# Performance work log

Measured on AMD Instinct MI355X. Metric: run time of the kernel, lower is better.

## Reference

```python
import jax, jax.numpy as jnp
import numpy as np

B, S, D = 4, 8192, 512


def log_g(x):
    # torch: where(x>=0, log(relu(x)+0.5), -softplus(-x)); relu(x)+0.5 >= 0.5 so log is safe
    return jnp.where(x >= 0, jnp.log(jax.nn.relu(x) + 0.5), -jax.nn.softplus(-x))


def parallel_scan_log(log_coeffs, log_values):
    # log_coeffs: (B,S,D); log_values: (B,S+1,D)
    a_star = jnp.pad(jnp.cumsum(log_coeffs, axis=1), ((0, 0), (1, 0), (0, 0)))  # (B,S+1,D)
    log_h = a_star + jax.lax.cumlogsumexp(log_values - a_star, axis=1)
    return jnp.exp(log_h)[:, 1:]  # (B,S,D)


def setup_inputs() -> dict:
    key = jax.random.key(0)
    ks = jax.random.split(key, 7)
    scale = 1.0 / np.sqrt(D)
    x = jax.random.normal(ks[0], (B, S, D), dtype=jnp.float32)
    pre_h = jnp.zeros((B, 1, D), dtype=jnp.float32)
    Wf = jax.random.normal(ks[1], (D, D), dtype=jnp.float32) * scale
    bf = jax.random.normal(ks[2], (D,), dtype=jnp.float32) * 0.01
    Wi = jax.random.normal(ks[3], (D, D), dtype=jnp.float32) * scale
    bi = jax.random.normal(ks[4], (D,), dtype=jnp.float32) * 0.01
    Wh = jax.random.normal(ks[5], (D, D), dtype=jnp.float32) * scale
    bh = jax.random.normal(ks[6], (D,), dtype=jnp.float32) * 0.01
    return {"x": x, "pre_h": pre_h, "Wf": Wf, "bf": bf, "Wi": Wi, "bi": bi, "Wh": Wh, "bh": bh}


def reference(x, pre_h, Wf, bf, Wi, bi, Wh, bh):
    # gates: log(sigmoid(k)) = -softplus(-k)
    log_f = -jax.nn.softplus(-(jnp.einsum('bsd,de->bse', x, Wf) + bf))
    log_i = -jax.nn.softplus(-(jnp.einsum('bsd,de->bse', x, Wi) + bi))
    log_tilde_h = log_g(jnp.einsum('bsd,de->bse', x, Wh) + bh)
    log_pre_h = log_g(pre_h)  # (B,1,D)
    log_values = jnp.concatenate([log_pre_h, log_i + log_tilde_h], axis=1)  # (B,S+1,D)
    return parallel_scan_log(log_f, log_values)
```

## Files before the change

### kernel.cpp

```cpp
#include <hip/hip_runtime.h>
#include <hip/hip_bf16.h>

#define BATCH 4
#define SEQ   8192
#define DIM   512
#define M_TOT (BATCH*SEQ)
#define NCHUNK 128
#define CLEN   64

#define GBM 128
#define GBN 128
#define GBK 64

typedef __attribute__((ext_vector_type(4))) int int4v;

__device__ __forceinline__ float sigmoidf_(float x) {
    return 1.0f / (1.0f + __expf(-x));
}
__device__ __forceinline__ float gfun_(float x) {
    return (x >= 0.0f) ? (x + 0.5f) : sigmoidf_(x);
}

__device__ __forceinline__ void stage16(const void* g, void* lds) {
    __builtin_amdgcn_global_load_lds((const __attribute__((address_space(1))) void*)g,
                                     (__attribute__((address_space(3))) void*)lds,
                                     16, 0, 0);
}

__global__ __launch_bounds__(256) void quant_x(const float* __restrict__ x,
                                               char* __restrict__ xh, char* __restrict__ xl)
{
    const int t = blockIdx.x * 256 + threadIdx.x;
    float4 v = ((const float4*)x)[t];
    float vals[4] = {v.x, v.y, v.z, v.w};
    char hs[4], ls[4];
    #pragma unroll
    for (int e = 0; e < 4; ++e) {
        float c = fminf(fmaxf(vals[e], -15.8f), 15.8f);
        int q = (int)rintf(c * 2048.0f);
        int hi = (q + 128) >> 8;
        int lo = q - (hi << 8);
        hs[e] = (char)hi; ls[e] = (char)lo;
    }
    char4 hv = {hs[0], hs[1], hs[2], hs[3]};
    char4 lv = {ls[0], ls[1], ls[2], ls[3]};
    *(char4*)&xh[(size_t)t * 4] = hv;
    *(char4*)&xl[(size_t)t * 4] = lv;
}

__global__ __launch_bounds__(256) void quant_wT(
    const float* __restrict__ Wf, const float* __restrict__ Wi, const float* __restrict__ Wh,
    char* __restrict__ wth, char* __restrict__ wtl)
{
    __shared__ float tile[64][65];
    const int g = blockIdx.z;
    const float* W = (g == 0) ? Wf : (g == 1) ? Wi : Wh;
    const int k0 = blockIdx.x * 64, n0 = blockIdx.y * 64;
    const int c = threadIdx.x & 63, r4 = threadIdx.x >> 6;
    #pragma unroll
    for (int p = 0; p < 16; ++p) {
        int r = p * 4 + r4;
        tile[r][c] = W[(size_t)(k0 + r) * DIM + n0 + c];
    }
    __syncthreads();
    const size_t gbase = (size_t)g * DIM * DIM;
    #pragma unroll
    for (int p = 0; p < 16; ++p) {
        int nr = p * 4 + r4;
        float w = tile[c][nr];
        float cl = fminf(fmaxf(w, -0.49f), 0.49f);
        int q = (int)rintf(cl * 65536.0f);
        int hi = (q + 128) >> 8;
        int lo = q - (hi << 8);
        size_t o = gbase + (size_t)(n0 + nr) * DIM + k0 + c;
        wth[o] = (char)hi;
        wtl[o] = (char)lo;
    }
}

__global__ __launch_bounds__(256, 2) void gemm_i8(
    const char* __restrict__ xh, const char* __restrict__ xl,
    const char* __restrict__ wth, const char* __restrict__ wtl,
    const float* __restrict__ bfv, const float* __restrict__ biv, const float* __restrict__ bhv,
    float* __restrict__ fb, float* __restrict__ sib, float* __restrict__ ghb)
{
    __shared__ char sA[2][GBM][GBK];
    __shared__ char sB[2][GBN][GBK];

    const int g  = blockIdx.x >> 2;
    const int n0 = (blockIdx.x & 3) * GBN;
    const int m0 = blockIdx.y * GBM;
    const int tid  = threadIdx.x;
    const int wave = tid >> 6;
    const int lane = tid & 63;
    const int wi = wave >> 1, wj = wave & 1;

    const char* wh_g = wth + (size_t)g * DIM * DIM;
    const char* wl_g = wtl + (size_t)g * DIM * DIM;

    int4v P2[4][4], P1[4][4];
    const int4v zero = {0, 0, 0, 0};
    #pragma unroll
    for (int i = 0; i < 4; ++i)
        #pragma unroll
        for (int j = 0; j < 4; ++j) { P2[i][j] = zero; P1[i][j] = zero; }

    for (int k0 = 0; k0 < DIM; k0 += GBK) {
        #pragma unroll
        for (int it = 0; it < 2; ++it) {
            const int grp = it * 4 + wave;
            const int m   = grp * 16 + (lane >> 2);
            const int kb  = (lane & 3) * 16;
            const int ksw = kb ^ (((m >> 1) & 3) << 4);
            char* ldsA = &sA[0][grp * 16][0];
            char* ldsB = &sB[0][grp * 16][0];
            char* ldsA1 = &sA[1][grp * 16][0];
            char* ldsB1 = &sB[1][grp * 16][0];
            stage16(xh  + (size_t)(m0 + m) * DIM + k0 + ksw, ldsA);
            stage16(xl  + (size_t)(m0 + m) * DIM + k0 + ksw, ldsA1);
            stage16(wh_g + (size_t)(n0 + m) * DIM + k0 + ksw, ldsB);
            stage16(wl_g + (size_t)(n0 + m) * DIM + k0 + ksw, ldsB1);
        }
        __syncthreads();

        const int kseg = (lane >> 4) * 16;
        int4v bhf[4], blf[4];
        #pragma unroll
        for (int j = 0; j < 4; ++j) {
            const int col = wj * 64 + j * 16 + (lane & 15);
            const int ks  = kseg ^ (((col >> 1) & 3) << 4);
            bhf[j] = *(const int4v*)&sB[0][col][ks];
            blf[j] = *(const int4v*)&sB[1][col][ks];
        }
        #pragma unroll
        for (int i = 0; i < 4; ++i) {
            const int row = wi * 64 + i * 16 + (lane & 15);
            const int ks  = kseg ^ (((row >> 1) & 3) << 4);
            int4v ahf = *(const int4v*)&sA[0][row][ks];
            int4v alf = *(const int4v*)&sA[1][row][ks];
            #pragma unroll
            for (int j = 0; j < 4; ++j) {
                P2[i][j] = __builtin_amdgcn_mfma_i32_16x16x64_i8(ahf, bhf[j], P2[i][j], 0, 0, 0);
                P1[i][j] = __builtin_amdgcn_mfma_i32_16x16x64_i8(ahf, blf[j], P1[i][j], 0, 0, 0);
                P1[i][j] = __builtin_amdgcn_mfma_i32_16x16x64_i8(alf, bhf[j], P1[i][j], 0, 0, 0);
            }
        }
        __syncthreads();
    }

    const float c2 = 1.0f / 2048.0f;
    const float c1 = 1.0f / 524288.0f;
    const float* bias = (g == 0) ? bfv : (g == 1) ? biv : bhv;
    float* outp = (g == 0) ? fb : (g == 1) ? sib : ghb;
    #pragma unroll
    for (int i = 0; i < 4; ++i) {
        #pragma unroll
        for (int j = 0; j < 4; ++j) {
            const int col = n0 + wj * 64 + j * 16 + (lane & 15);
            const float bv = bias[col];
            #pragma unroll
            for (int r = 0; r < 4; ++r) {
                const int row = m0 + wi * 64 + i * 16 + (lane >> 4) * 4 + r;
                float kv = (float)P2[i][j][r] * c2 + (float)P1[i][j][r] * c1 + bv;
                float o = (g == 2) ? gfun_(kv) : sigmoidf_(kv);
                outp[(size_t)row * DIM + col] = o;
            }
        }
    }
}

__global__ __launch_bounds__(256) void scan_pass1(
    const float* __restrict__ fb, const float* __restrict__ sib, const float* __restrict__ ghb,
    float* __restrict__ Ach, float* __restrict__ Bch)
{
    const int d = blockIdx.x * 256 + threadIdx.x;
    const int c = blockIdx.y;
    const int b = blockIdx.z;
    float A = 1.0f, Bacc = 0.0f;
    size_t base = ((size_t)(b * SEQ + c * CLEN)) * DIM + d;
    #pragma unroll 4
    for (int t = 0; t < CLEN; ++t) {
        float f = fb[base + (size_t)t * DIM];
        float v = sib[base + (size_t)t * DIM] * ghb[base + (size_t)t * DIM];
        Bacc = fmaf(f, Bacc, v);
        A *= f;
    }
    const int idx = (b * NCHUNK + c) * DIM + d;
    Ach[idx] = A;
    Bch[idx] = Bacc;
}

__global__ __launch_bounds__(256) void scan_pass2(
    const float* __restrict__ pre_h,
    const float* __restrict__ Ach, const float* __restrict__ Bch,
    float* __restrict__ carry)
{
    const int gidx = blockIdx.x * 256 + threadIdx.x;
    const int b = gidx >> 9;
    const int d = gidx & (DIM - 1);
    float h = gfun_(pre_h[b * DIM + d]);
    for (int c = 0; c < NCHUNK; ++c) {
        const int idx = (b * NCHUNK + c) * DIM + d;
        carry[idx] = h;
        h = fmaf(Ach[idx], h, Bch[idx]);
    }
}

__global__ __launch_bounds__(256) void scan_pass3(
    const float* __restrict__ fb, const float* __restrict__ sib, const float* __restrict__ ghb,
    const float* __restrict__ carry, float* __restrict__ out)
{
    const int d = blockIdx.x * 256 + threadIdx.x;
    const int c = blockIdx.y;
    const int b = blockIdx.z;
    float h = carry[(b * NCHUNK + c) * DIM + d];
    size_t base = ((size_t)(b * SEQ + c * CLEN)) * DIM + d;
    #pragma unroll 4
    for (int t = 0; t < CLEN; ++t) {
        float f = fb[base + (size_t)t * DIM];
        float v = sib[base + (size_t)t * DIM] * ghb[base + (size_t)t * DIM];
        h = fmaf(f, h, v);
        out[base + (size_t)t * DIM] = h;
    }
}

extern "C" void kernel_launch(void* const* d_in, const int* in_sizes, int n_in,
                              void* d_out, int out_size, void* d_ws, size_t ws_size,
                              hipStream_t stream) {
    const float* x     = (const float*)d_in[0];
    const float* pre_h = (const float*)d_in[1];
    const float* Wf    = (const float*)d_in[2];
    const float* bf    = (const float*)d_in[3];
    const float* Wi    = (const float*)d_in[4];
    const float* bi    = (const float*)d_in[5];
    const float* Wh    = (const float*)d_in[6];
    const float* bh    = (const float*)d_in[7];
    float* out = (float*)d_out;

    char* ws = (char*)d_ws;
    const size_t XQ = (size_t)M_TOT * DIM;
    const size_t WQ = (size_t)3 * DIM * DIM;
    const size_t FB = (size_t)M_TOT * DIM * sizeof(float);

    char*  xh  = ws;
    char*  xl  = ws + XQ;
    char*  wth = ws + 2 * XQ;
    char*  wtl = ws + 2 * XQ + WQ;
    float* fbuf  = (float*)(ws + 2 * XQ + 2 * WQ);
    float* sibuf = (float*)((char*)fbuf + FB);
    float* ghbuf = (float*)((char*)sibuf + FB);
    float* Ach   = (float*)((char*)ghbuf + FB);
    float* Bch   = (float*)((char*)Ach + (size_t)BATCH * NCHUNK * DIM * 4);
    float* carry = (float*)((char*)Bch + (size_t)BATCH * NCHUNK * DIM * 4);

    quant_x<<<(M_TOT * DIM / 4) / 256, 256, 0, stream>>>(x, xh, xl);
    quant_wT<<<dim3(8, 8, 3), 256, 0, stream>>>(Wf, Wi, Wh, wth, wtl);
    gemm_i8<<<dim3(12, M_TOT / GBM), 256, 0, stream>>>(
        xh, xl, wth, wtl, bf, bi, bh, fbuf, sibuf, ghbuf);
    scan_pass1<<<dim3(DIM / 256, NCHUNK, BATCH), 256, 0, stream>>>(fbuf, sibuf, ghbuf, Ach, Bch);
    scan_pass2<<<(BATCH * DIM) / 256, 256, 0, stream>>>(pre_h, Ach, Bch, carry);
    scan_pass3<<<dim3(DIM / 256, NCHUNK, BATCH), 256, 0, stream>>>(fbuf, sibuf, ghbuf, carry, out);
}
```

Measured before the change: 321.9 us.

## Fuse three gate GEMMs per tile and emit product buffer, double-buffer LDS

Each block now computes all three gate projections for one output tile in sequence. It keeps sigmoid(i) in registers and writes only f and the product v = sigmoid(i)*g(h) to global memory, so one full-size float intermediate buffer and its re-reads in both scan passes go away. The K loop gains LDS double buffering, with the next tile's global-to-LDS loads issued before the current tile's MFMAs, and a swizzled block index improves L2 reuse of X rows. In exchange, the 64 extra registers per thread may push register pressure past the 2-blocks-per-CU launch bound and cause spills. The LDS footprint also doubles to 64KB.

```diff
diff --git a/kernel.cpp b/kernel.cpp
--- a/kernel.cpp
+++ b/kernel.cpp
@@ -7,10 +7,6 @@
 #define M_TOT (BATCH*SEQ)
 #define NCHUNK 128
 #define CLEN   64
-
-#define GBM 128
-#define GBN 128
-#define GBK 64
 
 typedef __attribute__((ext_vector_type(4))) int int4v;
 
@@ -78,99 +74,129 @@
     }
 }
 
-__global__ __launch_bounds__(256, 2) void gemm_i8(
+__global__ __launch_bounds__(256, 2) void gemm_fused(
     const char* __restrict__ xh, const char* __restrict__ xl,
     const char* __restrict__ wth, const char* __restrict__ wtl,
     const float* __restrict__ bfv, const float* __restrict__ biv, const float* __restrict__ bhv,
-    float* __restrict__ fb, float* __restrict__ sib, float* __restrict__ ghb)
-{
-    __shared__ char sA[2][GBM][GBK];
-    __shared__ char sB[2][GBN][GBK];
-
-    const int g  = blockIdx.x >> 2;
-    const int n0 = (blockIdx.x & 3) * GBN;
-    const int m0 = blockIdx.y * GBM;
+    float* __restrict__ fb, float* __restrict__ vb)
+{
+    __shared__ char sA[2][2][128][64];
+    __shared__ char sB[2][2][128][64];
+
+    const int bid = blockIdx.x;
+    const int xr = bid & 7;
+    const int tt = bid >> 3;
+    const int n0 = (tt & 3) * 128;
+    const int m0 = (xr + 8 * (tt >> 2)) * 128;
+
     const int tid  = threadIdx.x;
     const int wave = tid >> 6;
     const int lane = tid & 63;
     const int wi = wave >> 1, wj = wave & 1;
 
-    const char* wh_g = wth + (size_t)g * DIM * DIM;
-    const char* wl_g = wtl + (size_t)g * DIM * DIM;
-
-    int4v P2[4][4], P1[4][4];
-    const int4v zero = {0, 0, 0, 0};
-    #pragma unroll
-    for (int i = 0; i < 4; ++i)
+    const float c2 = 1.0f / 2048.0f;
+    const float c1 = 1.0f / 524288.0f;
+
+    float si_r[4][4][4];
+
+    const int gorder[3] = {1, 2, 0};
+
+    #pragma unroll
+    for (int gi = 0; gi < 3; ++gi) {
+        const int g = gorder[gi];
+        const char* wh_g = wth + (size_t)g * DIM * DIM;
+        const char* wl_g = wtl + (size_t)g * DIM * DIM;
+
+        int4v P2[4][4], P1[4][4];
+        const int4v zero = {0, 0, 0, 0};
         #pragma unroll
-        for (int j = 0; j < 4; ++j) { P2[i][j] = zero; P1[i][j] = zero; }
-
-    for (int k0 = 0; k0 < DIM; k0 += GBK) {
+        for (int i = 0; i < 4; ++i)
+            #pragma unroll
+            for (int j = 0; j < 4; ++j) { P2[i][j] = zero; P1[i][j] = zero; }
+
         #pragma unroll
         for (int it = 0; it < 2; ++it) {
             const int grp = it * 4 + wave;
-            const int m   = grp * 16 + (lane >> 2);
+            const int mm  = grp * 16 + (lane >> 2);
             const int kb  = (lane & 3) * 16;
-            const int ksw = kb ^ (((m >> 1) & 3) << 4);
-            char* ldsA = &sA[0][grp * 16][0];
-            char* ldsB = &sB[0][grp * 16][0];
-            char* ldsA1 = &sA[1][grp * 16][0];
-            char* ldsB1 = &sB[1][grp * 16][0];
-            stage16(xh  + (size_t)(m0 + m) * DIM + k0 + ksw, ldsA);
-            stage16(xl  + (size_t)(m0 + m) * DIM + k0 + ksw, ldsA1);
-            stage16(wh_g + (size_t)(n0 + m) * DIM + k0 + ksw, ldsB);
-            stage16(wl_g + (size_t)(n0 + m) * DIM + k0 + ksw, ldsB1);
+            const int ksw = kb ^ (((mm >> 1) & 3) << 4);
+            stage16(xh   + (size_t)(m0 + mm) * DIM + ksw, &sA[0][0][grp * 16][0]);
+            stage16(xl   + (size_t)(m0 + mm) * DIM + ksw, &sA[0][1][grp * 16][0]);
+            stage16(wh_g + (size_t)(n0 + mm) * DIM + ksw, &sB[0][0][grp * 16][0]);
+            stage16(wl_g + (size_t)(n0 + mm) * DIM + ksw, &sB[0][1][grp * 16][0]);
         }
         __syncthreads();
 
-        const int kseg = (lane >> 4) * 16;
-        int4v bhf[4], blf[4];
-        #pragma unroll
-        for (int j = 0; j < 4; ++j) {
-            const int col = wj * 64 + j * 16 + (lane & 15);
-            const int ks  = kseg ^ (((col >> 1) & 3) << 4);
-            bhf[j] = *(const int4v*)&sB[0][col][ks];
-            blf[j] = *(const int4v*)&sB[1][col][ks];
+        for (int kt = 0; kt < 8; ++kt) {
+            const int cur = kt & 1;
+            if (kt < 7) {
+                const int nb = cur ^ 1;
+                const int k0 = (kt + 1) * 64;
+                #pragma unroll
+                for (int it = 0; it < 2; ++it) {
+                    const int grp = it * 4 + wave;
+                    const int mm  = grp * 16 + (lane >> 2);
+                    const int kb  = (lane & 3) * 16;
+                    const int ksw = kb ^ (((mm >> 1) & 3) << 4);
+                    stage16(xh   + (size_t)(m0 + mm) * DIM + k0 + ksw, &sA[nb][0][grp * 16][0]);
+                    stage16(xl   + (size_t)(m0 + mm) * DIM + k0 + ksw, &sA[nb][1][grp * 16][0]);
+                    stage16(wh_g + (size_t)(n0 + mm) * DIM + k0 + ksw, &sB[nb][0][grp * 16][0]);
+                    stage16(wl_g + (size_t)(n0 + mm) * DIM + k0 + ksw, &sB[nb][1][grp * 16][0]);
+                }
+            }
+            const int kseg = (lane >> 4) * 16;
+            int4v bhf[4], blf[4];
+            #pragma unroll
+            for (int j = 0; j < 4; ++j) {
+                const int col = wj * 64 + j * 16 + (lane & 15);
+                const int ks  = kseg ^ (((col >> 1) & 3) << 4);
+                bhf[j] = *(const int4v*)&sB[cur][0][col][ks];
+                blf[j] = *(const int4v*)&sB[cur][1][col][ks];
+            }
+            #pragma unroll
+            for (int i = 0; i < 4; ++i) {
+                const int row = wi * 64 + i * 16 + (lane & 15);
+                const int ks  = kseg ^ (((row >> 1) & 3) << 4);
+                int4v ahf = *(const int4v*)&sA[cur][0][row][ks];
+                int4v alf = *(const int4v*)&sA[cur][1][row][ks];
+                #pragma unroll
+                for (int j = 0; j < 4; ++j) {
+                    P2[i][j] = __builtin_amdgcn_mfma_i32_16x16x64_i8(ahf, bhf[j], P2[i][j], 0, 0, 0);
+                    P1[i][j] = __builtin_amdgcn_mfma_i32_16x16x64_i8(ahf, blf[j], P1[i][j], 0, 0, 0);
+                    P1[i][j] = __builtin_amdgcn_mfma_i32_16x16x64_i8(alf, bhf[j], P1[i][j], 0, 0, 0);
+                }
+            }
+            __syncthreads();
         }
-        #pragma unroll
-        for (int i = 0; i < 4; ++i) {
-            const int row = wi * 64 + i * 16 + (lane & 15);
-            const int ks  = kseg ^ (((row >> 1) & 3) << 4);
-            int4v ahf = *(const int4v*)&sA[0][row][ks];
-            int4v alf = *(const int4v*)&sA[1][row][ks];
-            #pragma unroll
-            for (int j = 0; j < 4; ++j) {
-                P2[i][j] = __builtin_amdgcn_mfma_i32_16x16x64_i8(ahf, bhf[j], P2[i][j], 0, 0, 0);
-                P1[i][j] = __builtin_amdgcn_mfma_i32_16x16x64_i8(ahf, blf[j], P1[i][j], 0, 0, 0);
-                P1[i][j] = __builtin_amdgcn_mfma_i32_16x16x64_i8(alf, bhf[j], P1[i][j], 0, 0, 0);
-            }
-        }
-        __syncthreads();
-    }
-
-    const float c2 = 1.0f / 2048.0f;
-    const float c1 = 1.0f / 524288.0f;
-    const float* bias = (g == 0) ? bfv : (g == 1) ? biv : bhv;
-    float* outp = (g == 0) ? fb : (g == 1) ? sib : ghb;
-    #pragma unroll
-    for (int i = 0; i < 4; ++i) {
+
+        const float* bias = (g == 0) ? bfv : (g == 1) ? biv : bhv;
         #pragma unroll
         for (int j = 0; j < 4; ++j) {
             const int col = n0 + wj * 64 + j * 16 + (lane & 15);
             const float bv = bias[col];
             #pragma unroll
-            for (int r = 0; r < 4; ++r) {
-                const int row = m0 + wi * 64 + i * 16 + (lane >> 4) * 4 + r;
-                float kv = (float)P2[i][j][r] * c2 + (float)P1[i][j][r] * c1 + bv;
-                float o = (g == 2) ? gfun_(kv) : sigmoidf_(kv);
-                outp[(size_t)row * DIM + col] = o;
+            for (int i = 0; i < 4; ++i) {
+                #pragma unroll
+                for (int r = 0; r < 4; ++r) {
+                    const float kv = (float)P2[i][j][r] * c2 + (float)P1[i][j][r] * c1 + bv;
+                    if (g == 1) {
+                        si_r[i][j][r] = sigmoidf_(kv);
+                    } else {
+                        const int row = m0 + wi * 64 + i * 16 + (lane >> 4) * 4 + r;
+                        if (g == 2) {
+                            vb[(size_t)row * DIM + col] = si_r[i][j][r] * gfun_(kv);
+                        } else {
+                            fb[(size_t)row * DIM + col] = sigmoidf_(kv);
+                        }
+                    }
+                }
             }
         }
     }
 }
 
 __global__ __launch_bounds__(256) void scan_pass1(
-    const float* __restrict__ fb, const float* __restrict__ sib, const float* __restrict__ ghb,
+    const float* __restrict__ fb, const float* __restrict__ vbuf,
     float* __restrict__ Ach, float* __restrict__ Bch)
 {
     const int d = blockIdx.x * 256 + threadIdx.x;
@@ -181,7 +207,7 @@
     #pragma unroll 4
     for (int t = 0; t < CLEN; ++t) {
         float f = fb[base + (size_t)t * DIM];
-        float v = sib[base + (size_t)t * DIM] * ghb[base + (size_t)t * DIM];
+        float v = vbuf[base + (size_t)t * DIM];
         Bacc = fmaf(f, Bacc, v);
         A *= f;
     }
@@ -207,7 +233,7 @@
 }
 
 __global__ __launch_bounds__(256) void scan_pass3(
-    const float* __restrict__ fb, const float* __restrict__ sib, const float* __restrict__ ghb,
+    const float* __restrict__ fb, const float* __restrict__ vbuf,
     const float* __restrict__ carry, float* __restrict__ out)
 {
     const int d = blockIdx.x * 256 + threadIdx.x;
@@ -218,7 +244,7 @@
     #pragma unroll 4
     for (int t = 0; t < CLEN; ++t) {
         float f = fb[base + (size_t)t * DIM];
-        float v = sib[base + (size_t)t * DIM] * ghb[base + (size_t)t * DIM];
+        float v = vbuf[base + (size_t)t * DIM];
         h = fmaf(f, h, v);
         out[base + (size_t)t * DIM] = h;
     }
@@ -241,23 +267,22 @@
     const size_t XQ = (size_t)M_TOT * DIM;
     const size_t WQ = (size_t)3 * DIM * DIM;
     const size_t FB = (size_t)M_TOT * DIM * sizeof(float);
+    const size_t CH = (size_t)BATCH * NCHUNK * DIM * sizeof(float);
 
     char*  xh  = ws;
     char*  xl  = ws + XQ;
     char*  wth = ws + 2 * XQ;
     char*  wtl = ws + 2 * XQ + WQ;
     float* fbuf  = (float*)(ws + 2 * XQ + 2 * WQ);
-    float* sibuf = (float*)((char*)fbuf + FB);
-    float* ghbuf = (float*)((char*)sibuf + FB);
-    float* Ach   = (float*)((char*)ghbuf + FB);
-    float* Bch   = (float*)((char*)Ach + (size_t)BATCH * NCHUNK * DIM * 4);
-    float* carry = (float*)((char*)Bch + (size_t)BATCH * NCHUNK * DIM * 4);
+    float* vbuf  = (float*)((char*)fbuf + FB);
+    float* Ach   = (float*)((char*)vbuf + FB);
+    float* Bch   = (float*)((char*)Ach + CH);
+    float* carry = (float*)((char*)Bch + CH);
 
     quant_x<<<(M_TOT * DIM / 4) / 256, 256, 0, stream>>>(x, xh, xl);
     quant_wT<<<dim3(8, 8, 3), 256, 0, stream>>>(Wf, Wi, Wh, wth, wtl);
-    gemm_i8<<<dim3(12, M_TOT / GBM), 256, 0, stream>>>(
-        xh, xl, wth, wtl, bf, bi, bh, fbuf, sibuf, ghbuf);
-    scan_pass1<<<dim3(DIM / 256, NCHUNK, BATCH), 256, 0, stream>>>(fbuf, sibuf, ghbuf, Ach, Bch);
+    gemm_fused<<<1024, 256, 0, stream>>>(xh, xl, wth, wtl, bf, bi, bh, fbuf, vbuf);
+    scan_pass1<<<dim3(DIM / 256, NCHUNK, BATCH), 256, 0, stream>>>(fbuf, vbuf, Ach, Bch);
     scan_pass2<<<(BATCH * DIM) / 256, 256, 0, stream>>>(pre_h, Ach, Bch, carry);
-    scan_pass3<<<dim3(DIM / 256, NCHUNK, BATCH), 256, 0, stream>>>(fbuf, sibuf, ghbuf, carry, out);
-}
+    scan_pass3<<<dim3(DIM / 256, NCHUNK, BATCH), 256, 0, stream>>>(fbuf, vbuf, carry, out);
+}
```

After: 392.5 us. 21.9% more time.
